# Performance work log

Hardware: AMD Instinct MI355X
Metric: run time of the kernel (lower is better)

## Reference

```python
import jax, jax.numpy as jnp
import numpy as np

N, E, F_IN, F_E = 50000, 800000, 128, 16
R, H, C = 4, 4, 32            # num_relations, heads, out_channels
HC = H * C                     # 128
NEG_SLOPE = 0.2                # PyG RGATConv default negative_slope
EPS = 1e-16                    # PyG softmax epsilon


def rgat_conv(x, src, dst, edge_type, edge_attr, w, q, k, e, le, b, concat):
    """Faithful PyG RGATConv (additive-self-attention, across-relation, dim=1, aggr=add).
    x: [N,F]; w: [R,F,H*C]; q,k,e: [H*C,H]; le: [F_e,H*C]; b: bias."""
    n = x.shape[0]
    xw = jnp.einsum('nf,rfo->rno', x, w)              # [R,N,H*C] per-relation projections
    x_i = xw[edge_type, dst]                          # [E,H*C] target-node proj per edge
    x_j = xw[edge_type, src]                          # [E,H*C] source-node proj per edge
    qi = x_i @ q                                      # [E,H]
    kj = x_j @ k + (edge_attr @ le) @ e               # [E,H] (edge features folded into keys)
    alpha = jax.nn.leaky_relu(qi + kj, NEG_SLOPE)     # [E,H]
    # softmax over incoming edges of each destination node (across relations)
    amax = jax.ops.segment_max(alpha, dst, num_segments=n)
    ex = jnp.exp(alpha - amax[dst])
    denom = jax.ops.segment_sum(ex, dst, num_segments=n)
    alpha = ex / (denom[dst] + EPS)
    msg = alpha[:, :, None] * x_j.reshape(-1, H, C)   # [E,H,C]
    out = jax.ops.segment_sum(msg, dst, num_segments=n)  # [N,H,C] sum aggregation
    out = out.reshape(n, H * C) if concat else out.mean(axis=1)
    return out + b


def setup_inputs() -> dict:
    key = jax.random.key(0)
    ks = jax.random.split(key, 18)
    p = 0.05
    inp = {
        'x': jax.random.normal(ks[0], (N, F_IN), dtype=jnp.float32),
        'edge_index': jax.random.randint(ks[1], (2, E), 0, N, dtype=jnp.int64)
            if jax.config.jax_enable_x64 else jax.random.randint(ks[1], (2, E), 0, N).astype(jnp.int32),
        'edge_attr': jax.random.normal(ks[2], (E, F_E), dtype=jnp.float32),
        'edge_type': jax.random.randint(ks[3], (E,), 0, R).astype(jnp.int32),
        # conv1 params (in=F_IN, concat=True -> bias of size H*C)
        'w1': jax.random.normal(ks[4], (R, F_IN, HC), dtype=jnp.float32) * p,
        'q1': jax.random.normal(ks[5], (HC, H), dtype=jnp.float32) * p,
        'k1': jax.random.normal(ks[6], (HC, H), dtype=jnp.float32) * p,
        'e1': jax.random.normal(ks[7], (HC, H), dtype=jnp.float32) * p,
        'le1': jax.random.normal(ks[8], (F_E, HC), dtype=jnp.float32) * p,
        'b1': jnp.zeros((HC,), dtype=jnp.float32),
        # conv3 params (in=H*C=128, concat=False -> bias of size C)
        'w3': jax.random.normal(ks[9], (R, HC, HC), dtype=jnp.float32) * p,
        'q3': jax.random.normal(ks[10], (HC, H), dtype=jnp.float32) * p,
        'k3': jax.random.normal(ks[11], (HC, H), dtype=jnp.float32) * p,
        'e3': jax.random.normal(ks[12], (HC, H), dtype=jnp.float32) * p,
        'le3': jax.random.normal(ks[13], (F_E, HC), dtype=jnp.float32) * p,
        'b3': jnp.zeros((C,), dtype=jnp.float32),
    }
    return inp


def reference(x, edge_index, edge_attr, edge_type,
              w1, q1, k1, e1, le1, b1,
              w3, q3, k3, e3, le3, b3):
    src, dst = edge_index[0], edge_index[1]
    h = jax.nn.relu(rgat_conv(x, src, dst, edge_type, edge_attr,
                              w1, q1, k1, e1, le1, b1, concat=True))
    out = rgat_conv(h, src, dst, edge_type, edge_attr,
                    w3, q3, k3, e3, le3, b3, concat=False)
    return out
```

## Files before the change

### kernel.cpp

```cpp
#include <hip/hip_runtime.h>


#define NEG_SLOPE 0.2f
#define SOFT_EPS 1e-16f

typedef __attribute__((ext_vector_type(8))) short bf16x8;
typedef __attribute__((ext_vector_type(4))) float f32x4;
typedef __attribute__((ext_vector_type(4))) unsigned short u16x4;
typedef __attribute__((ext_vector_type(4))) _Float16 half4;
typedef __attribute__((ext_vector_type(8))) _Float16 half8;

__device__ __forceinline__ void bf16split(float f, unsigned short& h, unsigned short& l) {
  unsigned u = __float_as_uint(f);
  unsigned r = u + 0x7FFFu + ((u >> 16) & 1u);
  h = (unsigned short)(r >> 16);
  float fh = __uint_as_float(((unsigned)h) << 16);
  float d = f - fh;
  unsigned u2 = __float_as_uint(d);
  unsigned r2 = u2 + 0x7FFFu + ((u2 >> 16) & 1u);
  l = (unsigned short)(r2 >> 16);
}


__device__ __forceinline__ void hist_body(int id, const int* __restrict__ dst,
                                          int* __restrict__ deg, int E) {
  int e = id * 256 + (int)threadIdx.x;
  if (e < E) atomicAdd(&deg[dst[e]], 1);
}

__device__ __forceinline__ void convx_body(int id, const float* __restrict__ in,
                                           unsigned short* __restrict__ hi,
                                           unsigned short* __restrict__ lo, int total8) {
  int i = id * 256 + (int)threadIdx.x;
  if (i >= total8) return;
  const float4* p = (const float4*)in + (size_t)i * 2;
  float4 a = p[0], b = p[1];
  float v[8] = {a.x, a.y, a.z, a.w, b.x, b.y, b.z, b.w};
  bf16x8 hv, lv;
#pragma unroll
  for (int j = 0; j < 8; ++j) {
    unsigned short h, l;
    bf16split(v[j], h, l);
    hv[j] = (short)h; lv[j] = (short)l;
  }
  *(bf16x8*)(hi + (size_t)i * 8) = hv;
  *(bf16x8*)(lo + (size_t)i * 8) = lv;
}

__device__ __forceinline__ void convw_body(int idx, const float* __restrict__ w1,
                                           const float* __restrict__ w3,
                                           unsigned short* __restrict__ wF1h,
                                           unsigned short* __restrict__ wF1l,
                                           unsigned short* __restrict__ wF3h,
                                           unsigned short* __restrict__ wF3l) {
  if (idx >= 131072) return;
  int L = idx >> 16;
  int rem = idx & 65535;
  int r = rem >> 14, rem2 = rem & 16383, f = rem2 >> 7, o = rem2 & 127;
  const float* w = L ? w3 : w1;
  unsigned short* dh = L ? wF3h : wF1h;
  unsigned short* dl = L ? wF3l : wF1l;
  float v = w[(r * 128 + f) * 128 + o];
  unsigned short h, l;
  bf16split(v, h, l);
  int ot = o >> 4, c = o & 15, kc = f >> 5, q = (f >> 3) & 3, j = f & 7;
  int di = r * 16384 + ((((ot * 4 + kc) * 4 + q) * 16 + c) * 8 + j);
  dh[di] = h;
  dl[di] = l;
}

__device__ __forceinline__ void wqk_body(int idx, const float* __restrict__ w1,
                                         const float* __restrict__ q1, const float* __restrict__ k1,
                                         const float* __restrict__ w3, const float* __restrict__ q3,
                                         const float* __restrict__ k3, float* __restrict__ wqk) {
  if (idx >= 8192) return;
  int L = idx >> 12, rem = idx & 4095;
  int r = rem >> 10, rem2 = rem & 1023, f = rem2 >> 3, j = rem2 & 7;
  const float* w = L ? w3 : w1;
  const float* qk = (j < 4) ? (L ? q3 : q1) : (L ? k3 : k1);
  int h = j & 3;
  const float* wrow = w + (r * 128 + f) * 128;
  float acc = 0.f;
  for (int o = 0; o < 128; ++o) acc += wrow[o] * qk[o * 4 + h];
  wqk[idx] = acc;
}

__device__ __forceinline__ void lee_body(const float* __restrict__ le1, const float* __restrict__ e1,
                                         const float* __restrict__ le3, const float* __restrict__ e3,
                                         float* __restrict__ lee) {
  int t = threadIdx.x;
  if (t >= 128) return;
  const float* le = (t < 64) ? le1 : le3;
  const float* ee = (t < 64) ? e1 : e3;
  int u = t & 63, f = u >> 2, h = u & 3;
  float acc = 0.f;
  for (int o = 0; o < 128; ++o) acc += le[f * 128 + o] * ee[o * 4 + h];
  lee[t] = acc;
}

__global__ __launch_bounds__(256) void pre_kernel(
    const int* __restrict__ dst, int* __restrict__ deg, int E,
    const float* __restrict__ x, unsigned short* __restrict__ xhi,
    unsigned short* __restrict__ xlo, int total8,
    const float* __restrict__ w1, const float* __restrict__ q1, const float* __restrict__ k1,
    const float* __restrict__ w3, const float* __restrict__ q3, const float* __restrict__ k3,
    float* __restrict__ wqk,
    const float* __restrict__ le1, const float* __restrict__ e1,
    const float* __restrict__ le3, const float* __restrict__ e3, float* __restrict__ lee,
    unsigned short* __restrict__ wF1h, unsigned short* __restrict__ wF1l,
    unsigned short* __restrict__ wF3h, unsigned short* __restrict__ wF3l,
    int nAB, int eb, int cxb) {
  int bid = blockIdx.x;
  if (bid < nAB) {
    int id = bid >> 1;
    if (bid & 1) {
      if (id < eb) hist_body(id, dst, deg, E);
    } else {
      if (id < cxb) convx_body(id, x, xhi, xlo, total8);
    }
  } else {
    int b2 = bid - nAB;
    if (b2 < 512) {
      convw_body(b2 * 256 + (int)threadIdx.x, w1, w3, wF1h, wF1l, wF3h, wF3l);
    } else if (b2 < 544) {
      wqk_body((b2 - 512) * 256 + (int)threadIdx.x, w1, q1, k1, w3, q3, k3, wqk);
    } else {
      lee_body(le1, e1, le3, e3, lee);
    }
  }
}


__global__ __launch_bounds__(256) void scanA_kernel(const int* __restrict__ deg,
                                                    int* __restrict__ bsum, int N) {
  int b = blockIdx.x, t = threadIdx.x;
  int base = b * 1024 + t * 4;
  int s = 0;
#pragma unroll
  for (int j = 0; j < 4; ++j) {
    int i = base + j;
    if (i < N) s += deg[i];
  }
#pragma unroll
  for (int o = 1; o < 64; o <<= 1) s += __shfl_xor(s, o);
  __shared__ int wsum[4];
  if ((t & 63) == 0) wsum[t >> 6] = s;
  __syncthreads();
  if (t == 0) bsum[b] = wsum[0] + wsum[1] + wsum[2] + wsum[3];
}

__global__ __launch_bounds__(256) void scanB_kernel(const int* __restrict__ bsum,
                                                    int* __restrict__ boff,
                                                    int* __restrict__ row_start,
                                                    int nb, int N) {
  int t = threadIdx.x;
  int v = (t < nb) ? bsum[t] : 0;
  int inc = v;
#pragma unroll
  for (int o = 1; o < 64; o <<= 1) {
    int u = __shfl_up(inc, o);
    if ((t & 63) >= o) inc += u;
  }
  __shared__ int wt[4];
  if ((t & 63) == 63) wt[t >> 6] = inc;
  __syncthreads();
  int add = 0;
  for (int wv = 0; wv < (t >> 6); ++wv) add += wt[wv];
  inc += add;
  if (t < nb) boff[t] = inc - v;
  if (t == 255) row_start[N] = inc;
}

__global__ __launch_bounds__(256) void scanC_kernel(const int* __restrict__ deg,
                                                    const int* __restrict__ boff,
                                                    int* __restrict__ row_start,
                                                    int* __restrict__ cursor, int N) {
  int b = blockIdx.x, t = threadIdx.x;
  int base = b * 1024 + t * 4;
  int d[4];
  int s = 0;
#pragma unroll
  for (int j = 0; j < 4; ++j) {
    int i = base + j;
    d[j] = (i < N) ? deg[i] : 0;
    s += d[j];
  }
  int inc = s;
#pragma unroll
  for (int o = 1; o < 64; o <<= 1) {
    int u = __shfl_up(inc, o);
    if ((t & 63) >= o) inc += u;
  }
  __shared__ int wt[4];
  if ((t & 63) == 63) wt[t >> 6] = inc;
  __syncthreads();
  int add = boff[b];
  for (int wv = 0; wv < (t >> 6); ++wv) add += wt[wv];
  int off = add + inc - s;
#pragma unroll
  for (int j = 0; j < 4; ++j) {
    int i = base + j;
    if (i < N) {
      row_start[i] = off;
      cursor[i] = off;
      off += d[j];
    }
  }
}


__device__ __forceinline__ void scatter_body(int id, const int* __restrict__ src,
                                             const int* __restrict__ dst,
                                             const int* __restrict__ et,
                                             int* __restrict__ cursor,
                                             int4* __restrict__ es, int E) {
  int e = id * 256 + (int)threadIdx.x;
  if (e >= E) return;
  int d = dst[e];
  int pos = atomicAdd(&cursor[d], 1);
  es[pos] = make_int4(src[e], d, et[e], e);
}

__device__ __forceinline__ void qkx_body(int nbid, char* smem, const float* __restrict__ xin,
                                         const float* __restrict__ wqk, float* __restrict__ qn,
                                         float* __restrict__ kn, int N) {
  float* swqk = (float*)smem;
  int t = threadIdx.x;
#pragma unroll
  for (int j = 0; j < 16; ++j) {
    int i = j * 256 + t;
    swqk[(i >> 10) * 1032 + (i & 1023)] = wqk[i];
  }
  __syncthreads();
  int nb = nbid * 64;
  int rl = t >> 2, r = t & 3;
  int n = nb + rl;
  int nc = n < N ? n : N - 1;
  const float4* xr = (const float4*)(xin + (size_t)nc * 128);
  const float* wb = swqk + r * 1032;
  float aq0 = 0, aq1 = 0, aq2 = 0, aq3 = 0;
  float ak0 = 0, ak1 = 0, ak2 = 0, ak3 = 0;
#pragma unroll 4
  for (int f4 = 0; f4 < 32; ++f4) {
    float4 xv = xr[f4];
    const float* w0 = wb + f4 * 32;
    float4 qa = *(const float4*)(w0);
    float4 ka = *(const float4*)(w0 + 4);
    float4 qb = *(const float4*)(w0 + 8);
    float4 kb = *(const float4*)(w0 + 12);
    float4 qc = *(const float4*)(w0 + 16);
    float4 kc = *(const float4*)(w0 + 20);
    float4 qd = *(const float4*)(w0 + 24);
    float4 kd = *(const float4*)(w0 + 28);
    aq0 += xv.x * qa.x + xv.y * qb.x + xv.z * qc.x + xv.w * qd.x;
    aq1 += xv.x * qa.y + xv.y * qb.y + xv.z * qc.y + xv.w * qd.y;
    aq2 += xv.x * qa.z + xv.y * qb.z + xv.z * qc.z + xv.w * qd.z;
    aq3 += xv.x * qa.w + xv.y * qb.w + xv.z * qc.w + xv.w * qd.w;
    ak0 += xv.x * ka.x + xv.y * kb.x + xv.z * kc.x + xv.w * kd.x;
    ak1 += xv.x * ka.y + xv.y * kb.y + xv.z * kc.y + xv.w * kd.y;
    ak2 += xv.x * ka.z + xv.y * kb.z + xv.z * kc.z + xv.w * kd.z;
    ak3 += xv.x * ka.w + xv.y * kb.w + xv.z * kc.w + xv.w * kd.w;
  }
  if (n < N) {
    *(float4*)(qn + ((size_t)r * N + n) * 4) = make_float4(aq0, aq1, aq2, aq3);
    *(float4*)(kn + ((size_t)r * N + n) * 4) = make_float4(ak0, ak1, ak2, ak3);
  }
}

__device__ __forceinline__ void proj_body(int pid, char* smem,
                                          const unsigned short* __restrict__ xhi,
                                          const unsigned short* __restrict__ xlo,
                                          const unsigned short* __restrict__ wFh,
                                          const unsigned short* __restrict__ wFl,
                                          _Float16* __restrict__ xwh, int N) {
  bf16x8* wl_h = (bf16x8*)smem;
  bf16x8* wl_l = wl_h + 1024;
  int r = pid & 3;
  int h0 = (pid >> 2) & 1;
  int nb = (pid >> 3) * 128;
  int t = threadIdx.x;
  const bf16x8* srcH = (const bf16x8*)(wFh + r * 16384) + h0 * 1024;
  const bf16x8* srcL = (const bf16x8*)(wFl + r * 16384) + h0 * 1024;
#pragma unroll
  for (int j = 0; j < 4; ++j) {
    int i = j * 256 + t;
    wl_h[i] = srcH[i];
    wl_l[i] = srcL[i];
  }
  __syncthreads();

  int wv = t >> 6;
  int lane = t & 63;
  int c = lane & 15, q = lane >> 4;
  int nodebase = nb + wv * 32;
  int n0 = nodebase + c;
  int n1 = nodebase + 16 + c;
  int n0c = n0 < N ? n0 : N - 1;
  int n1c = n1 < N ? n1 : N - 1;

  f32x4 acc[4][2];
#pragma unroll
  for (int ot = 0; ot < 4; ++ot)
#pragma unroll
    for (int nt = 0; nt < 2; ++nt) acc[ot][nt] = (f32x4){0.f, 0.f, 0.f, 0.f};

  bf16x8 xb[2][4];
  {
    int k0 = q * 8;
    xb[0][0] = *(const bf16x8*)(xhi + (size_t)n0c * 128 + k0);
    xb[0][1] = *(const bf16x8*)(xlo + (size_t)n0c * 128 + k0);
    xb[0][2] = *(const bf16x8*)(xhi + (size_t)n1c * 128 + k0);
    xb[0][3] = *(const bf16x8*)(xlo + (size_t)n1c * 128 + k0);
  }
#pragma unroll
  for (int kc = 0; kc < 4; ++kc) {
    if (kc < 3) {
      int k0 = (kc + 1) * 32 + q * 8;
      xb[(kc + 1) & 1][0] = *(const bf16x8*)(xhi + (size_t)n0c * 128 + k0);
      xb[(kc + 1) & 1][1] = *(const bf16x8*)(xlo + (size_t)n0c * 128 + k0);
      xb[(kc + 1) & 1][2] = *(const bf16x8*)(xhi + (size_t)n1c * 128 + k0);
      xb[(kc + 1) & 1][3] = *(const bf16x8*)(xlo + (size_t)n1c * 128 + k0);
    }
    bf16x8 b0h = xb[kc & 1][0], b0l = xb[kc & 1][1];
    bf16x8 b1h = xb[kc & 1][2], b1l = xb[kc & 1][3];
#pragma unroll
    for (int ot = 0; ot < 4; ++ot) {
      int fi = ((ot * 4 + kc) * 4 + q) * 16 + c;
      bf16x8 ah = wl_h[fi];
      bf16x8 al = wl_l[fi];
      acc[ot][0] = __builtin_amdgcn_mfma_f32_16x16x32_bf16(ah, b0h, acc[ot][0], 0, 0, 0);
      acc[ot][0] = __builtin_amdgcn_mfma_f32_16x16x32_bf16(ah, b0l, acc[ot][0], 0, 0, 0);
      acc[ot][0] = __builtin_amdgcn_mfma_f32_16x16x32_bf16(al, b0h, acc[ot][0], 0, 0, 0);
      acc[ot][1] = __builtin_amdgcn_mfma_f32_16x16x32_bf16(ah, b1h, acc[ot][1], 0, 0, 0);
      acc[ot][1] = __builtin_amdgcn_mfma_f32_16x16x32_bf16(ah, b1l, acc[ot][1], 0, 0, 0);
      acc[ot][1] = __builtin_amdgcn_mfma_f32_16x16x32_bf16(al, b1h, acc[ot][1], 0, 0, 0);
    }
  }

#pragma unroll
  for (int nt = 0; nt < 2; ++nt) {
    int n = nodebase + nt * 16 + c;
    if (n < N) {
      _Float16* basep = xwh + ((size_t)r * N + n) * 128 + h0 * 64 + q * 4;
#pragma unroll
      for (int ot = 0; ot < 4; ++ot) {
        f32x4 a = acc[ot][nt];
        half4 hv;
        hv[0] = (_Float16)a.x; hv[1] = (_Float16)a.y;
        hv[2] = (_Float16)a.z; hv[3] = (_Float16)a.w;
        *(half4*)(basep + ot * 16) = hv;
      }
    }
  }
}

__global__ __launch_bounds__(256) void sc9_kernel(
    const int* __restrict__ src, const int* __restrict__ dst, const int* __restrict__ et,
    int* __restrict__ cursor, int4* __restrict__ es, int E,
    const float* __restrict__ xin, const float* __restrict__ wqk,
    float* __restrict__ qn, float* __restrict__ kn, int N, int qxb,
    const unsigned short* __restrict__ xhi, const unsigned short* __restrict__ xlo,
    const unsigned short* __restrict__ wFh, const unsigned short* __restrict__ wFl,
    _Float16* __restrict__ xwh, int pjb) {
  extern __shared__ char smem[];
  int bid = blockIdx.x;
  int g = bid / 9, r9 = bid - g * 9;
  if (r9 < 4) {
    scatter_body(g * 4 + r9, src, dst, et, cursor, es, E);
  } else if (r9 == 4) {
    if (g < qxb) qkx_body(g, smem, xin, wqk, qn, kn, N);
  } else {
    int id = g * 4 + (r9 - 5);
    if (id < pjb) proj_body(id, smem, xhi, xlo, wFh, wFl, xwh, N);
  }
}


__global__ __launch_bounds__(256) void ek2_kernel(
    const int4* __restrict__ es, const float* __restrict__ ea,
    const float* __restrict__ lee, float* __restrict__ eks1,
    float* __restrict__ eks3, int E) {
  __shared__ float sl[128];
  if (threadIdx.x < 128) sl[threadIdx.x] = lee[threadIdx.x];
  __syncthreads();
  int i = blockIdx.x * 256 + (int)threadIdx.x;
  if (i >= E) return;
  int eid = es[i].w;
  const float4* a4 = (const float4*)(ea + (size_t)eid * 16);
  float a1[4] = {0, 0, 0, 0}, a3[4] = {0, 0, 0, 0};
#pragma unroll
  for (int ii = 0; ii < 4; ++ii) {
    float4 v = a4[ii];
    int f = ii * 4;
#pragma unroll
    for (int h = 0; h < 4; ++h) {
      a1[h] += v.x * sl[f * 4 + h] + v.y * sl[(f + 1) * 4 + h] +
               v.z * sl[(f + 2) * 4 + h] + v.w * sl[(f + 3) * 4 + h];
      a3[h] += v.x * sl[64 + f * 4 + h] + v.y * sl[64 + (f + 1) * 4 + h] +
               v.z * sl[64 + (f + 2) * 4 + h] + v.w * sl[64 + (f + 3) * 4 + h];
    }
  }
  *(float4*)(eks1 + (size_t)i * 4) = make_float4(a1[0], a1[1], a1[2], a1[3]);
  *(float4*)(eks3 + (size_t)i * 4) = make_float4(a3[0], a3[1], a3[2], a3[3]);
}

__global__ __launch_bounds__(256) void p2_kernel(
    const unsigned short* __restrict__ xhi, const unsigned short* __restrict__ xlo,
    const unsigned short* __restrict__ wFh, const unsigned short* __restrict__ wFl,
    _Float16* __restrict__ xwh, int N,
    const float* __restrict__ xin, const float* __restrict__ wqk,
    float* __restrict__ qn, float* __restrict__ kn, int pjb, int qxb) {
  extern __shared__ char smem[];
  int bid = blockIdx.x;
  int g = bid / 5, r5 = bid - g * 5;
  if (r5 == 4) {
    if (g < qxb) qkx_body(g, smem, xin, wqk, qn, kn, N);
  } else {
    int id = g * 4 + r5;
    if (id < pjb) proj_body(id, smem, xhi, xlo, wFh, wFl, xwh, N);
  }
}


__device__ __forceinline__ float4 edge_alpha(const int4* __restrict__ es,
                                             const float* __restrict__ qn,
                                             const float* __restrict__ kn,
                                             const float* __restrict__ eks,
                                             int i, int d, int N) {
  int4 v = es[i];
  float4 kv = *(const float4*)(kn + (v.z * N + v.x) * 4);
  float4 ev = ((const float4*)eks)[i];
  float4 q4 = *(const float4*)(qn + (v.z * N + d) * 4);
  float4 a = make_float4(q4.x + kv.x + ev.x, q4.y + kv.y + ev.y,
                         q4.z + kv.z + ev.z, q4.w + kv.w + ev.w);
  a.x = a.x > 0.f ? a.x : NEG_SLOPE * a.x;
  a.y = a.y > 0.f ? a.y : NEG_SLOPE * a.y;
  a.z = a.z > 0.f ? a.z : NEG_SLOPE * a.z;
  a.w = a.w > 0.f ? a.w : NEG_SLOPE * a.w;
  return a;
}

__device__ __forceinline__ float4 max4(float4 a, float4 b) {
  return make_float4(fmaxf(a.x, b.x), fmaxf(a.y, b.y), fmaxf(a.z, b.z), fmaxf(a.w, b.w));
}

__global__ __launch_bounds__(256) void agg_kernel(
    const int4* __restrict__ es, const int* __restrict__ row_start,
    const float* __restrict__ qn, const float* __restrict__ kn,
    const float* __restrict__ eks, float* __restrict__ alpha_s,
    const _Float16* __restrict__ xwh, const float* __restrict__ bias,
    float* __restrict__ out, unsigned short* __restrict__ xhi,
    unsigned short* __restrict__ xlo, int N, int concat) {
  int d = blockIdx.x * 16 + (threadIdx.x >> 4);
  if (d >= N) return;
  int ql = threadIdx.x & 15;
  int rs = row_start[d], re = row_start[d + 1];
  int deg = re - rs;
  int h = ql >> 2;

  float acc[8];
#pragma unroll
  for (int j = 0; j < 8; ++j) acc[j] = 0.f;
  float rden = 0.f;

  if (deg > 0) {
    float4 m = make_float4(-1e30f, -1e30f, -1e30f, -1e30f);
    float4 ar0 = m, ar1 = m, ar2 = m, ar3 = m;
    bool fast = (deg <= 64);
    bool v0 = ql < deg, v1 = 16 + ql < deg, v2 = 32 + ql < deg, v3 = 48 + ql < deg;
    if (fast) {
      int dm1 = deg - 1;
      int o0 = v0 ? ql : dm1;
      int o1 = v1 ? 16 + ql : dm1;
      int o2 = v2 ? 32 + ql : dm1;
      int o3 = v3 ? 48 + ql : dm1;
      float4 a0 = edge_alpha(es, qn, kn, eks, rs + o0, d, N);
      float4 a1 = edge_alpha(es, qn, kn, eks, rs + o1, d, N);
      float4 a2 = edge_alpha(es, qn, kn, eks, rs + o2, d, N);
      float4 a3 = edge_alpha(es, qn, kn, eks, rs + o3, d, N);
      if (v0) { ar0 = a0; m = max4(m, a0); }
      if (v1) { ar1 = a1; m = max4(m, a1); }
      if (v2) { ar2 = a2; m = max4(m, a2); }
      if (v3) { ar3 = a3; m = max4(m, a3); }
    } else {
      for (int i = rs + ql; i < re; i += 16) {
        float4 a = edge_alpha(es, qn, kn, eks, i, d, N);
        ((float4*)alpha_s)[i] = a;
        m = max4(m, a);
      }
    }
#pragma unroll
    for (int o = 1; o < 16; o <<= 1) {
      m.x = fmaxf(m.x, __shfl_xor(m.x, o));
      m.y = fmaxf(m.y, __shfl_xor(m.y, o));
      m.z = fmaxf(m.z, __shfl_xor(m.z, o));
      m.w = fmaxf(m.w, __shfl_xor(m.w, o));
    }

    float4 s = make_float4(0.f, 0.f, 0.f, 0.f);
    if (fast) {
#define SWEEPB(V, AR, OFF)                                                   \
      if (V) {                                                               \
        float4 e4 = make_float4(__expf(AR.x - m.x), __expf(AR.y - m.y),      \
                                __expf(AR.z - m.z), __expf(AR.w - m.w));     \
        ((float4*)alpha_s)[rs + OFF + ql] = e4;                              \
        s.x += e4.x; s.y += e4.y; s.z += e4.z; s.w += e4.w;                  \
      }
      SWEEPB(v0, ar0, 0)
      SWEEPB(v1, ar1, 16)
      SWEEPB(v2, ar2, 32)
      SWEEPB(v3, ar3, 48)
#undef SWEEPB
    } else {
      for (int i = rs + ql; i < re; i += 16) {
        float4 a = ((const float4*)alpha_s)[i];
        float4 e4 = make_float4(__expf(a.x - m.x), __expf(a.y - m.y),
                                __expf(a.z - m.z), __expf(a.w - m.w));
        ((float4*)alpha_s)[i] = e4;
        s.x += e4.x; s.y += e4.y; s.z += e4.z; s.w += e4.w;
      }
    }
#pragma unroll
    for (int o = 1; o < 16; o <<= 1) {
      s.x += __shfl_xor(s.x, o); s.y += __shfl_xor(s.y, o);
      s.z += __shfl_xor(s.z, o); s.w += __shfl_xor(s.w, o);
    }
    float smh = (h == 0) ? s.x : (h == 1) ? s.y : (h == 2) ? s.z : s.w;
    rden = 1.f / (smh + SOFT_EPS);

    int e = rs;
    for (; e + 4 <= re; e += 4) {
      int4 a0 = es[e];
      int4 a1 = es[e + 1];
      int4 a2 = es[e + 2];
      int4 a3 = es[e + 3];
      float w0 = alpha_s[e * 4 + h];
      float w1 = alpha_s[(e + 1) * 4 + h];
      float w2 = alpha_s[(e + 2) * 4 + h];
      float w3 = alpha_s[(e + 3) * 4 + h];
      half8 x0 = *(const half8*)(xwh + (a0.z * N + a0.x) * 128 + ql * 8);
      half8 x1 = *(const half8*)(xwh + (a1.z * N + a1.x) * 128 + ql * 8);
      half8 x2 = *(const half8*)(xwh + (a2.z * N + a2.x) * 128 + ql * 8);
      half8 x3 = *(const half8*)(xwh + (a3.z * N + a3.x) * 128 + ql * 8);
#pragma unroll
      for (int j = 0; j < 8; ++j) {
        acc[j] = fmaf((float)x0[j], w0, acc[j]);
        acc[j] = fmaf((float)x1[j], w1, acc[j]);
        acc[j] = fmaf((float)x2[j], w2, acc[j]);
        acc[j] = fmaf((float)x3[j], w3, acc[j]);
      }
    }
    for (; e < re; ++e) {
      int4 a0 = es[e];
      float w0 = alpha_s[e * 4 + h];
      half8 x0 = *(const half8*)(xwh + (a0.z * N + a0.x) * 128 + ql * 8);
#pragma unroll
      for (int j = 0; j < 8; ++j) acc[j] = fmaf((float)x0[j], w0, acc[j]);
    }
  }
#pragma unroll
  for (int j = 0; j < 8; ++j) acc[j] *= rden;

  if (concat) {
    float4 b0 = ((const float4*)bias)[ql * 2];
    float4 b1 = ((const float4*)bias)[ql * 2 + 1];
    float v[8] = {acc[0] + b0.x, acc[1] + b0.y, acc[2] + b0.z, acc[3] + b0.w,
                  acc[4] + b1.x, acc[5] + b1.y, acc[6] + b1.z, acc[7] + b1.w};
    u16x4 hv0, lv0, hv1, lv1;
#pragma unroll
    for (int j = 0; j < 8; ++j) {
      v[j] = v[j] > 0.f ? v[j] : 0.f;
      unsigned short hh, ll;
      bf16split(v[j], hh, ll);
      if (j < 4) { hv0[j] = hh; lv0[j] = ll; }
      else { hv1[j - 4] = hh; lv1[j - 4] = ll; }
    }
    float* orow = out + (size_t)d * 128 + ql * 8;
    *(float4*)orow = make_float4(v[0], v[1], v[2], v[3]);
    *(float4*)(orow + 4) = make_float4(v[4], v[5], v[6], v[7]);
    *(u16x4*)(xhi + (size_t)d * 128 + ql * 8) = hv0;
    *(u16x4*)(xhi + (size_t)d * 128 + ql * 8 + 4) = hv1;
    *(u16x4*)(xlo + (size_t)d * 128 + ql * 8) = lv0;
    *(u16x4*)(xlo + (size_t)d * 128 + ql * 8 + 4) = lv1;
  } else {
#pragma unroll
    for (int j = 0; j < 8; ++j) {
      acc[j] += __shfl_xor(acc[j], 4);
      acc[j] += __shfl_xor(acc[j], 8);
    }
    if (ql < 4) {
      float4 b0 = ((const float4*)bias)[ql * 2];
      float4 b1 = ((const float4*)bias)[ql * 2 + 1];
      float* orow = out + (size_t)d * 32 + ql * 8;
      *(float4*)orow = make_float4(0.25f * acc[0] + b0.x, 0.25f * acc[1] + b0.y,
                                   0.25f * acc[2] + b0.z, 0.25f * acc[3] + b0.w);
      *(float4*)(orow + 4) = make_float4(0.25f * acc[4] + b1.x, 0.25f * acc[5] + b1.y,
                                         0.25f * acc[6] + b1.z, 0.25f * acc[7] + b1.w);
    }
  }
}

extern "C" void kernel_launch(void* const* d_in, const int* in_sizes, int n_in,
                              void* d_out, int out_size, void* d_ws, size_t ws_size,
                              hipStream_t stream) {
  const float* x   = (const float*)d_in[0];
  const int*   ei  = (const int*)d_in[1];
  const float* ea  = (const float*)d_in[2];
  const int*   etp = (const int*)d_in[3];
  const float* w1  = (const float*)d_in[4];
  const float* q1  = (const float*)d_in[5];
  const float* k1  = (const float*)d_in[6];
  const float* e1  = (const float*)d_in[7];
  const float* le1 = (const float*)d_in[8];
  const float* b1  = (const float*)d_in[9];
  const float* w3  = (const float*)d_in[10];
  const float* q3  = (const float*)d_in[11];
  const float* k3  = (const float*)d_in[12];
  const float* e3  = (const float*)d_in[13];
  const float* le3 = (const float*)d_in[14];
  const float* b3  = (const float*)d_in[15];
  const int N = in_sizes[0] / 128;
  const int E = in_sizes[3];
  const int* srcp = ei;
  const int* dstp = ei + E;

  float* ws   = (float*)d_ws;
  _Float16* xwh = (_Float16*)ws;
  float* qn   = ws + (size_t)2 * N * 128;
  float* kn   = qn + (size_t)4 * N * 4;
  float* eks1 = kn + (size_t)4 * N * 4;
  float* eks3 = eks1 + (size_t)E * 4;
  float* alph = eks3 + (size_t)E * 4;
  float* hbuf = alph + (size_t)E * 4;
  float* leeb = hbuf + (size_t)N * 128;
  float* wqkb = leeb + 128;
  int* deg      = (int*)(wqkb + 8192);
  int* rowst    = deg + N;
  int* cursor   = rowst + N + 1;
  int* bsum     = cursor + N;
  int* boff     = bsum + 256;
  uintptr_t pe = (uintptr_t)(boff + 256);
  pe = (pe + 15) & ~(uintptr_t)15;
  int4* es      = (int4*)pe;
  uintptr_t pa = (uintptr_t)(es + E);
  pa = (pa + 255) & ~(uintptr_t)255;
  unsigned short* xhi  = (unsigned short*)pa;
  unsigned short* xlo  = xhi + (size_t)N * 128;
  unsigned short* wF1h = xlo + (size_t)N * 128;
  unsigned short* wF1l = wF1h + 4 * 128 * 128;
  unsigned short* wF3h = wF1l + 4 * 128 * 128;
  unsigned short* wF3l = wF3h + 4 * 128 * 128;
  (void)ws_size; (void)n_in; (void)out_size;

  int eb   = (E + 255) / 256;
  int nb16 = (N + 15) / 16;
  int nbs  = (N + 1023) / 1024;
  int pgy  = (N + 127) / 128;
  int pjb  = 8 * pgy;
  int qxb  = (N + 63) / 64;
  int cxb  = (N * 128 / 8 + 255) / 256;

  hipMemsetAsync(deg, 0, (size_t)N * sizeof(int), stream);

  int M = eb > cxb ? eb : cxb;
  int nAB = 2 * M;
  int preg = nAB + 512 + 32 + 1;
  pre_kernel<<<preg, 256, 0, stream>>>(dstp, deg, E, x, xhi, xlo, N * 128 / 8,
                                       w1, q1, k1, w3, q3, k3, wqkb,
                                       le1, e1, le3, e3, leeb,
                                       wF1h, wF1l, wF3h, wF3l, nAB, eb, cxb);
  scanA_kernel<<<nbs, 256, 0, stream>>>(deg, bsum, N);
  scanB_kernel<<<1, 256, 0, stream>>>(bsum, boff, rowst, nbs, N);
  scanC_kernel<<<nbs, 256, 0, stream>>>(deg, boff, rowst, cursor, N);

  int scq = (eb + 3) / 4;
  int pjq = (pjb + 3) / 4;
  int g9 = scq;
  if (qxb > g9) g9 = qxb;
  if (pjq > g9) g9 = pjq;
  sc9_kernel<<<9 * g9, 256, 32768, stream>>>(srcp, dstp, etp, cursor, es, E,
                                             x, wqkb, qn, kn, N, qxb,
                                             xhi, xlo, wF1h, wF1l, xwh, pjb);

  ek2_kernel<<<eb, 256, 0, stream>>>(es, ea, leeb, eks1, eks3, E);

  agg_kernel<<<nb16, 256, 0, stream>>>(es, rowst, qn, kn, eks1, alph, xwh,
                                       b1, hbuf, xhi, xlo, N, 1);

  int p2grp = pjq > qxb ? pjq : qxb;
  p2_kernel<<<5 * p2grp, 256, 32768, stream>>>(xhi, xlo, wF3h, wF3l, xwh, N,
                                               hbuf, wqkb + 4096, qn, kn, pjb, qxb);

  agg_kernel<<<nb16, 256, 0, stream>>>(es, rowst, qn, kn, eks3, alph, xwh,
                                       b3, (float*)d_out, xhi, xlo, N, 0);
}
```

Before: 432.2 us.

## Compute edge keys in original order in pre-kernel and pack sorted edge records

The edge-feature key projection now runs inside the pre kernel, indexed by original edge id, and the separate ek2 kernel and its gather through the sorted edge list are gone. Sorted edge records shrink from int4 to int2, with edge type packed into the top bits of the source index alongside the original edge id. This cuts one launch and halves the edge-list bytes read by the aggregation kernels. The cost is that aggregation now reads eks indirectly by edge id, which is a random access where it used to be sequential, and every pre-kernel block recomputes the small le·e table.

```diff
diff --git a/kernel.cpp b/kernel.cpp
--- a/kernel.cpp
+++ b/kernel.cpp
@@ -3,6 +3,7 @@
 
 #define NEG_SLOPE 0.2f
 #define SOFT_EPS 1e-16f
+#define SRC_MASK 0x07FFFFFF
 
 typedef __attribute__((ext_vector_type(8))) short bf16x8;
 typedef __attribute__((ext_vector_type(4))) float f32x4;
@@ -45,6 +46,42 @@
   }
   *(bf16x8*)(hi + (size_t)i * 8) = hv;
   *(bf16x8*)(lo + (size_t)i * 8) = lv;
+}
+
+__device__ __forceinline__ void ekp_body(int id, const float* __restrict__ ea,
+                                         const float* __restrict__ le1, const float* __restrict__ e1,
+                                         const float* __restrict__ le3, const float* __restrict__ e3,
+                                         float* __restrict__ eks1, float* __restrict__ eks3,
+                                         int E) {
+  __shared__ float sl[128];
+  int t = threadIdx.x;
+  if (t < 128) {
+    const float* le = (t < 64) ? le1 : le3;
+    const float* ee = (t < 64) ? e1 : e3;
+    int u = t & 63, f = u >> 2, h = u & 3;
+    float acc = 0.f;
+    for (int o = 0; o < 128; ++o) acc += le[f * 128 + o] * ee[o * 4 + h];
+    sl[t] = acc;
+  }
+  __syncthreads();
+  int i = id * 256 + t;
+  if (i >= E) return;
+  const float4* a4 = (const float4*)(ea + (size_t)i * 16);
+  float a1[4] = {0, 0, 0, 0}, a3[4] = {0, 0, 0, 0};
+#pragma unroll
+  for (int ii = 0; ii < 4; ++ii) {
+    float4 v = a4[ii];
+    int f = ii * 4;
+#pragma unroll
+    for (int h = 0; h < 4; ++h) {
+      a1[h] += v.x * sl[f * 4 + h] + v.y * sl[(f + 1) * 4 + h] +
+               v.z * sl[(f + 2) * 4 + h] + v.w * sl[(f + 3) * 4 + h];
+      a3[h] += v.x * sl[64 + f * 4 + h] + v.y * sl[64 + (f + 1) * 4 + h] +
+               v.z * sl[64 + (f + 2) * 4 + h] + v.w * sl[64 + (f + 3) * 4 + h];
+    }
+  }
+  *(float4*)(eks1 + (size_t)i * 4) = make_float4(a1[0], a1[1], a1[2], a1[3]);
+  *(float4*)(eks3 + (size_t)i * 4) = make_float4(a3[0], a3[1], a3[2], a3[3]);
 }
 
 __device__ __forceinline__ void convw_body(int idx, const float* __restrict__ w1,
@@ -85,47 +122,36 @@
   wqk[idx] = acc;
 }
 
-__device__ __forceinline__ void lee_body(const float* __restrict__ le1, const float* __restrict__ e1,
-                                         const float* __restrict__ le3, const float* __restrict__ e3,
-                                         float* __restrict__ lee) {
-  int t = threadIdx.x;
-  if (t >= 128) return;
-  const float* le = (t < 64) ? le1 : le3;
-  const float* ee = (t < 64) ? e1 : e3;
-  int u = t & 63, f = u >> 2, h = u & 3;
-  float acc = 0.f;
-  for (int o = 0; o < 128; ++o) acc += le[f * 128 + o] * ee[o * 4 + h];
-  lee[t] = acc;
-}
-
 __global__ __launch_bounds__(256) void pre_kernel(
     const int* __restrict__ dst, int* __restrict__ deg, int E,
     const float* __restrict__ x, unsigned short* __restrict__ xhi,
     unsigned short* __restrict__ xlo, int total8,
+    const float* __restrict__ ea,
+    const float* __restrict__ le1, const float* __restrict__ e1,
+    const float* __restrict__ le3, const float* __restrict__ e3,
+    float* __restrict__ eks1, float* __restrict__ eks3,
     const float* __restrict__ w1, const float* __restrict__ q1, const float* __restrict__ k1,
     const float* __restrict__ w3, const float* __restrict__ q3, const float* __restrict__ k3,
     float* __restrict__ wqk,
-    const float* __restrict__ le1, const float* __restrict__ e1,
-    const float* __restrict__ le3, const float* __restrict__ e3, float* __restrict__ lee,
     unsigned short* __restrict__ wF1h, unsigned short* __restrict__ wF1l,
     unsigned short* __restrict__ wF3h, unsigned short* __restrict__ wF3l,
-    int nAB, int eb, int cxb) {
+    int nABC, int eb, int cxb) {
   int bid = blockIdx.x;
-  if (bid < nAB) {
-    int id = bid >> 1;
-    if (bid & 1) {
+  if (bid < nABC) {
+    int id = bid / 3, r3 = bid - id * 3;
+    if (r3 == 0) {
       if (id < eb) hist_body(id, dst, deg, E);
+    } else if (r3 == 1) {
+      if (id < cxb) convx_body(id, x, xhi, xlo, total8);
     } else {
-      if (id < cxb) convx_body(id, x, xhi, xlo, total8);
+      if (id < eb) ekp_body(id, ea, le1, e1, le3, e3, eks1, eks3, E);
     }
   } else {
-    int b2 = bid - nAB;
+    int b2 = bid - nABC;
     if (b2 < 512) {
       convw_body(b2 * 256 + (int)threadIdx.x, w1, w3, wF1h, wF1l, wF3h, wF3l);
-    } else if (b2 < 544) {
+    } else {
       wqk_body((b2 - 512) * 256 + (int)threadIdx.x, w1, q1, k1, w3, q3, k3, wqk);
-    } else {
-      lee_body(le1, e1, le3, e3, lee);
     }
   }
 }
@@ -213,12 +239,12 @@
                                              const int* __restrict__ dst,
                                              const int* __restrict__ et,
                                              int* __restrict__ cursor,
-                                             int4* __restrict__ es, int E) {
+                                             int2* __restrict__ es2, int E) {
   int e = id * 256 + (int)threadIdx.x;
   if (e >= E) return;
   int d = dst[e];
   int pos = atomicAdd(&cursor[d], 1);
-  es[pos] = make_int4(src[e], d, et[e], e);
+  es2[pos] = make_int2(src[e] | (et[e] << 27), e);
 }
 
 __device__ __forceinline__ void qkx_body(int nbid, char* smem, const float* __restrict__ xin,
@@ -356,7 +382,7 @@
 
 __global__ __launch_bounds__(256) void sc9_kernel(
     const int* __restrict__ src, const int* __restrict__ dst, const int* __restrict__ et,
-    int* __restrict__ cursor, int4* __restrict__ es, int E,
+    int* __restrict__ cursor, int2* __restrict__ es2, int E,
     const float* __restrict__ xin, const float* __restrict__ wqk,
     float* __restrict__ qn, float* __restrict__ kn, int N, int qxb,
     const unsigned short* __restrict__ xhi, const unsigned short* __restrict__ xlo,
@@ -366,42 +392,13 @@
   int bid = blockIdx.x;
   int g = bid / 9, r9 = bid - g * 9;
   if (r9 < 4) {
-    scatter_body(g * 4 + r9, src, dst, et, cursor, es, E);
+    scatter_body(g * 4 + r9, src, dst, et, cursor, es2, E);
   } else if (r9 == 4) {
     if (g < qxb) qkx_body(g, smem, xin, wqk, qn, kn, N);
   } else {
     int id = g * 4 + (r9 - 5);
     if (id < pjb) proj_body(id, smem, xhi, xlo, wFh, wFl, xwh, N);
   }
-}
-
-
-__global__ __launch_bounds__(256) void ek2_kernel(
-    const int4* __restrict__ es, const float* __restrict__ ea,
-    const float* __restrict__ lee, float* __restrict__ eks1,
-    float* __restrict__ eks3, int E) {
-  __shared__ float sl[128];
-  if (threadIdx.x < 128) sl[threadIdx.x] = lee[threadIdx.x];
-  __syncthreads();
-  int i = blockIdx.x * 256 + (int)threadIdx.x;
-  if (i >= E) return;
-  int eid = es[i].w;
-  const float4* a4 = (const float4*)(ea + (size_t)eid * 16);
-  float a1[4] = {0, 0, 0, 0}, a3[4] = {0, 0, 0, 0};
-#pragma unroll
-  for (int ii = 0; ii < 4; ++ii) {
-    float4 v = a4[ii];
-    int f = ii * 4;
-#pragma unroll
-    for (int h = 0; h < 4; ++h) {
-      a1[h] += v.x * sl[f * 4 + h] + v.y * sl[(f + 1) * 4 + h] +
-               v.z * sl[(f + 2) * 4 + h] + v.w * sl[(f + 3) * 4 + h];
-      a3[h] += v.x * sl[64 + f * 4 + h] + v.y * sl[64 + (f + 1) * 4 + h] +
-               v.z * sl[64 + (f + 2) * 4 + h] + v.w * sl[64 + (f + 3) * 4 + h];
-    }
-  }
-  *(float4*)(eks1 + (size_t)i * 4) = make_float4(a1[0], a1[1], a1[2], a1[3]);
-  *(float4*)(eks3 + (size_t)i * 4) = make_float4(a3[0], a3[1], a3[2], a3[3]);
 }
 
 __global__ __launch_bounds__(256) void p2_kernel(
@@ -422,15 +419,17 @@
 }
 
 
-__device__ __forceinline__ float4 edge_alpha(const int4* __restrict__ es,
+__device__ __forceinline__ float4 edge_alpha(const int2* __restrict__ es2,
                                              const float* __restrict__ qn,
                                              const float* __restrict__ kn,
                                              const float* __restrict__ eks,
                                              int i, int d, int N) {
-  int4 v = es[i];
-  float4 kv = *(const float4*)(kn + (v.z * N + v.x) * 4);
-  float4 ev = ((const float4*)eks)[i];
-  float4 q4 = *(const float4*)(qn + (v.z * N + d) * 4);
+  int2 v = es2[i];
+  int et = (int)((unsigned)v.x >> 27);
+  int sn = v.x & SRC_MASK;
+  float4 kv = *(const float4*)(kn + (et * N + sn) * 4);
+  float4 ev = ((const float4*)eks)[v.y];
+  float4 q4 = *(const float4*)(qn + (et * N + d) * 4);
   float4 a = make_float4(q4.x + kv.x + ev.x, q4.y + kv.y + ev.y,
                          q4.z + kv.z + ev.z, q4.w + kv.w + ev.w);
   a.x = a.x > 0.f ? a.x : NEG_SLOPE * a.x;
@@ -445,7 +444,7 @@
 }
 
 __global__ __launch_bounds__(256) void agg_kernel(
-    const int4* __restrict__ es, const int* __restrict__ row_start,
+    const int2* __restrict__ es2, const int* __restrict__ row_start,
     const float* __restrict__ qn, const float* __restrict__ kn,
     const float* __restrict__ eks, float* __restrict__ alpha_s,
     const _Float16* __restrict__ xwh, const float* __restrict__ bias,
@@ -474,17 +473,17 @@
       int o1 = v1 ? 16 + ql : dm1;
       int o2 = v2 ? 32 + ql : dm1;
       int o3 = v3 ? 48 + ql : dm1;
-      float4 a0 = edge_alpha(es, qn, kn, eks, rs + o0, d, N);
-      float4 a1 = edge_alpha(es, qn, kn, eks, rs + o1, d, N);
-      float4 a2 = edge_alpha(es, qn, kn, eks, rs + o2, d, N);
-      float4 a3 = edge_alpha(es, qn, kn, eks, rs + o3, d, N);
+      float4 a0 = edge_alpha(es2, qn, kn, eks, rs + o0, d, N);
+      float4 a1 = edge_alpha(es2, qn, kn, eks, rs + o1, d, N);
+      float4 a2 = edge_alpha(es2, qn, kn, eks, rs + o2, d, N);
+      float4 a3 = edge_alpha(es2, qn, kn, eks, rs + o3, d, N);
       if (v0) { ar0 = a0; m = max4(m, a0); }
       if (v1) { ar1 = a1; m = max4(m, a1); }
       if (v2) { ar2 = a2; m = max4(m, a2); }
       if (v3) { ar3 = a3; m = max4(m, a3); }
     } else {
       for (int i = rs + ql; i < re; i += 16) {
-        float4 a = edge_alpha(es, qn, kn, eks, i, d, N);
+        float4 a = edge_alpha(es2, qn, kn, eks, i, d, N);
         ((float4*)alpha_s)[i] = a;
         m = max4(m, a);
       }
@@ -530,18 +529,22 @@
 
     int e = rs;
     for (; e + 4 <= re; e += 4) {
-      int4 a0 = es[e];
-      int4 a1 = es[e + 1];
-      int4 a2 = es[e + 2];
-      int4 a3 = es[e + 3];
+      int2 a0 = es2[e];
+      int2 a1 = es2[e + 1];
+      int2 a2 = es2[e + 2];
+      int2 a3 = es2[e + 3];
       float w0 = alpha_s[e * 4 + h];
       float w1 = alpha_s[(e + 1) * 4 + h];
       float w2 = alpha_s[(e + 2) * 4 + h];
       float w3 = alpha_s[(e + 3) * 4 + h];
-      half8 x0 = *(const half8*)(xwh + (a0.z * N + a0.x) * 128 + ql * 8);
-      half8 x1 = *(const half8*)(xwh + (a1.z * N + a1.x) * 128 + ql * 8);
-      half8 x2 = *(const half8*)(xwh + (a2.z * N + a2.x) * 128 + ql * 8);
-      half8 x3 = *(const half8*)(xwh + (a3.z * N + a3.x) * 128 + ql * 8);
+      int p0 = ((int)((unsigned)a0.x >> 27)) * N + (a0.x & SRC_MASK);
+      int p1 = ((int)((unsigned)a1.x >> 27)) * N + (a1.x & SRC_MASK);
+      int p2 = ((int)((unsigned)a2.x >> 27)) * N + (a2.x & SRC_MASK);
+      int p3 = ((int)((unsigned)a3.x >> 27)) * N + (a3.x & SRC_MASK);
+      half8 x0 = *(const half8*)(xwh + (size_t)p0 * 128 + ql * 8);
+      half8 x1 = *(const half8*)(xwh + (size_t)p1 * 128 + ql * 8);
+      half8 x2 = *(const half8*)(xwh + (size_t)p2 * 128 + ql * 8);
+      half8 x3 = *(const half8*)(xwh + (size_t)p3 * 128 + ql * 8);
 #pragma unroll
       for (int j = 0; j < 8; ++j) {
         acc[j] = fmaf((float)x0[j], w0, acc[j]);
@@ -551,9 +554,10 @@
       }
     }
     for (; e < re; ++e) {
-      int4 a0 = es[e];
+      int2 a0 = es2[e];
       float w0 = alpha_s[e * 4 + h];
-      half8 x0 = *(const half8*)(xwh + (a0.z * N + a0.x) * 128 + ql * 8);
+      int p0 = ((int)((unsigned)a0.x >> 27)) * N + (a0.x & SRC_MASK);
+      half8 x0 = *(const half8*)(xwh + (size_t)p0 * 128 + ql * 8);
 #pragma unroll
       for (int j = 0; j < 8; ++j) acc[j] = fmaf((float)x0[j], w0, acc[j]);
     }
@@ -632,8 +636,7 @@
   float* eks3 = eks1 + (size_t)E * 4;
   float* alph = eks3 + (size_t)E * 4;
   float* hbuf = alph + (size_t)E * 4;
-  float* leeb = hbuf + (size_t)N * 128;
-  float* wqkb = leeb + 128;
+  float* wqkb = hbuf + (size_t)N * 128;
   int* deg      = (int*)(wqkb + 8192);
   int* rowst    = deg + N;
   int* cursor   = rowst + N + 1;
@@ -641,8 +644,8 @@
   int* boff     = bsum + 256;
   uintptr_t pe = (uintptr_t)(boff + 256);
   pe = (pe + 15) & ~(uintptr_t)15;
-  int4* es      = (int4*)pe;
-  uintptr_t pa = (uintptr_t)(es + E);
+  int2* es2     = (int2*)pe;
+  uintptr_t pa = (uintptr_t)(es2 + E);
   pa = (pa + 255) & ~(uintptr_t)255;
   unsigned short* xhi  = (unsigned short*)pa;
   unsigned short* xlo  = xhi + (size_t)N * 128;
@@ -663,12 +666,12 @@
   hipMemsetAsync(deg, 0, (size_t)N * sizeof(int), stream);
 
   int M = eb > cxb ? eb : cxb;
-  int nAB = 2 * M;
-  int preg = nAB + 512 + 32 + 1;
+  int nABC = 3 * M;
+  int preg = nABC + 512 + 32;
   pre_kernel<<<preg, 256, 0, stream>>>(dstp, deg, E, x, xhi, xlo, N * 128 / 8,
+                                       ea, le1, e1, le3, e3, eks1, eks3,
                                        w1, q1, k1, w3, q3, k3, wqkb,
-                                       le1, e1, le3, e3, leeb,
-                                       wF1h, wF1l, wF3h, wF3l, nAB, eb, cxb);
+                                       wF1h, wF1l, wF3h, wF3l, nABC, eb, cxb);
   scanA_kernel<<<nbs, 256, 0, stream>>>(deg, bsum, N);
   scanB_kernel<<<1, 256, 0, stream>>>(bsum, boff, rowst, nbs, N);
   scanC_kernel<<<nbs, 256, 0, stream>>>(deg, boff, rowst, cursor, N);
@@ -678,19 +681,17 @@
   int g9 = scq;
   if (qxb > g9) g9 = qxb;
   if (pjq > g9) g9 = pjq;
-  sc9_kernel<<<9 * g9, 256, 32768, stream>>>(srcp, dstp, etp, cursor, es, E,
+  sc9_kernel<<<9 * g9, 256, 32768, stream>>>(srcp, dstp, etp, cursor, es2, E,
                                              x, wqkb, qn, kn, N, qxb,
                                              xhi, xlo, wF1h, wF1l, xwh, pjb);
 
-  ek2_kernel<<<eb, 256, 0, stream>>>(es, ea, leeb, eks1, eks3, E);
-
-  agg_kernel<<<nb16, 256, 0, stream>>>(es, rowst, qn, kn, eks1, alph, xwh,
+  agg_kernel<<<nb16, 256, 0, stream>>>(es2, rowst, qn, kn, eks1, alph, xwh,
                                        b1, hbuf, xhi, xlo, N, 1);
 
   int p2grp = pjq > qxb ? pjq : qxb;
   p2_kernel<<<5 * p2grp, 256, 32768, stream>>>(xhi, xlo, wF3h, wF3l, xwh, N,
                                                hbuf, wqkb + 4096, qn, kn, pjb, qxb);
 
-  agg_kernel<<<nb16, 256, 0, stream>>>(es, rowst, qn, kn, eks3, alph, xwh,
+  agg_kernel<<<nb16, 256, 0, stream>>>(es2, rowst, qn, kn, eks3, alph, xwh,
                                        b3, (float*)d_out, xhi, xlo, N, 0);
 }
```

Measured after the change: 436.5 us. No clear change (+1.0%).

## Fuse layer-2 attention q/k projection into layer-1 aggregation epilogue

Applied to the files above, without the earlier changes.

The per-node q/k attention logits for the second layer are now computed inside the first aggregation kernel's epilogue, using in-register activations and a 16-lane shuffle reduction per relation. This removes the fp32 hidden-buffer write and the separate qkx blocks in the second projection kernel, which becomes a plain projection launch. It writes into new qn2/kn2 buffers so the first-layer logits are not overwritten while still being read. In exchange the aggregation epilogue does more arithmetic and shuffles per node, and its weight loads may raise register pressure.

```diff
diff --git a/kernel.cpp b/kernel.cpp
--- a/kernel.cpp
+++ b/kernel.cpp
@@ -404,21 +404,13 @@
   *(float4*)(eks3 + (size_t)i * 4) = make_float4(a3[0], a3[1], a3[2], a3[3]);
 }
 
-__global__ __launch_bounds__(256) void p2_kernel(
+__global__ __launch_bounds__(256) void projL2_kernel(
     const unsigned short* __restrict__ xhi, const unsigned short* __restrict__ xlo,
     const unsigned short* __restrict__ wFh, const unsigned short* __restrict__ wFl,
-    _Float16* __restrict__ xwh, int N,
-    const float* __restrict__ xin, const float* __restrict__ wqk,
-    float* __restrict__ qn, float* __restrict__ kn, int pjb, int qxb) {
+    _Float16* __restrict__ xwh, int N, int pjb) {
   extern __shared__ char smem[];
-  int bid = blockIdx.x;
-  int g = bid / 5, r5 = bid - g * 5;
-  if (r5 == 4) {
-    if (g < qxb) qkx_body(g, smem, xin, wqk, qn, kn, N);
-  } else {
-    int id = g * 4 + r5;
-    if (id < pjb) proj_body(id, smem, xhi, xlo, wFh, wFl, xwh, N);
-  }
+  int id = blockIdx.x;
+  if (id < pjb) proj_body(id, smem, xhi, xlo, wFh, wFl, xwh, N);
 }
 
 
@@ -450,7 +442,9 @@
     const float* __restrict__ eks, float* __restrict__ alpha_s,
     const _Float16* __restrict__ xwh, const float* __restrict__ bias,
     float* __restrict__ out, unsigned short* __restrict__ xhi,
-    unsigned short* __restrict__ xlo, int N, int concat) {
+    unsigned short* __restrict__ xlo,
+    float* __restrict__ qn2, float* __restrict__ kn2,
+    const float* __restrict__ wqk3, int N, int concat) {
   int d = blockIdx.x * 16 + (threadIdx.x >> 4);
   if (d >= N) return;
   int ql = threadIdx.x & 15;
@@ -575,13 +569,37 @@
       if (j < 4) { hv0[j] = hh; lv0[j] = ll; }
       else { hv1[j - 4] = hh; lv1[j - 4] = ll; }
     }
-    float* orow = out + (size_t)d * 128 + ql * 8;
-    *(float4*)orow = make_float4(v[0], v[1], v[2], v[3]);
-    *(float4*)(orow + 4) = make_float4(v[4], v[5], v[6], v[7]);
     *(u16x4*)(xhi + (size_t)d * 128 + ql * 8) = hv0;
     *(u16x4*)(xhi + (size_t)d * 128 + ql * 8 + 4) = hv1;
     *(u16x4*)(xlo + (size_t)d * 128 + ql * 8) = lv0;
     *(u16x4*)(xlo + (size_t)d * 128 + ql * 8 + 4) = lv1;
+
+#pragma unroll
+    for (int r = 0; r < 4; ++r) {
+      const float* wb = wqk3 + r * 1024 + ql * 64;
+      float p0 = 0, p1 = 0, p2 = 0, p3 = 0, p4 = 0, p5 = 0, p6 = 0, p7 = 0;
+#pragma unroll
+      for (int j = 0; j < 8; ++j) {
+        float hv = v[j];
+        float4 wa = *(const float4*)(wb + j * 8);
+        float4 wk = *(const float4*)(wb + j * 8 + 4);
+        p0 = fmaf(hv, wa.x, p0); p1 = fmaf(hv, wa.y, p1);
+        p2 = fmaf(hv, wa.z, p2); p3 = fmaf(hv, wa.w, p3);
+        p4 = fmaf(hv, wk.x, p4); p5 = fmaf(hv, wk.y, p5);
+        p6 = fmaf(hv, wk.z, p6); p7 = fmaf(hv, wk.w, p7);
+      }
+#pragma unroll
+      for (int o = 1; o < 16; o <<= 1) {
+        p0 += __shfl_xor(p0, o); p1 += __shfl_xor(p1, o);
+        p2 += __shfl_xor(p2, o); p3 += __shfl_xor(p3, o);
+        p4 += __shfl_xor(p4, o); p5 += __shfl_xor(p5, o);
+        p6 += __shfl_xor(p6, o); p7 += __shfl_xor(p7, o);
+      }
+      if (ql == 0) {
+        *(float4*)(qn2 + ((size_t)r * N + d) * 4) = make_float4(p0, p1, p2, p3);
+        *(float4*)(kn2 + ((size_t)r * N + d) * 4) = make_float4(p4, p5, p6, p7);
+      }
+    }
   } else {
 #pragma unroll
     for (int j = 0; j < 8; ++j) {
@@ -628,11 +646,12 @@
   _Float16* xwh = (_Float16*)ws;
   float* qn   = ws + (size_t)2 * N * 128;
   float* kn   = qn + (size_t)4 * N * 4;
-  float* eks1 = kn + (size_t)4 * N * 4;
+  float* qn2  = kn + (size_t)4 * N * 4;
+  float* kn2  = qn2 + (size_t)4 * N * 4;
+  float* eks1 = kn2 + (size_t)4 * N * 4;
   float* eks3 = eks1 + (size_t)E * 4;
   float* alph = eks3 + (size_t)E * 4;
-  float* hbuf = alph + (size_t)E * 4;
-  float* leeb = hbuf + (size_t)N * 128;
+  float* leeb = alph + (size_t)E * 4;
   float* wqkb = leeb + 128;
   int* deg      = (int*)(wqkb + 8192);
   int* rowst    = deg + N;
@@ -685,12 +704,12 @@
   ek2_kernel<<<eb, 256, 0, stream>>>(es, ea, leeb, eks1, eks3, E);
 
   agg_kernel<<<nb16, 256, 0, stream>>>(es, rowst, qn, kn, eks1, alph, xwh,
-                                       b1, hbuf, xhi, xlo, N, 1);
-
-  int p2grp = pjq > qxb ? pjq : qxb;
-  p2_kernel<<<5 * p2grp, 256, 32768, stream>>>(xhi, xlo, wF3h, wF3l, xwh, N,
-                                               hbuf, wqkb + 4096, qn, kn, pjb, qxb);
-
-  agg_kernel<<<nb16, 256, 0, stream>>>(es, rowst, qn, kn, eks3, alph, xwh,
-                                       b3, (float*)d_out, xhi, xlo, N, 0);
-}
+                                       b1, (float*)d_out, xhi, xlo,
+                                       qn2, kn2, wqkb + 4096, N, 1);
+
+  projL2_kernel<<<pjb, 256, 32768, stream>>>(xhi, xlo, wF3h, wF3l, xwh, N, pjb);
+
+  agg_kernel<<<nb16, 256, 0, stream>>>(es, rowst, qn2, kn2, eks3, alph, xwh,
+                                       b3, (float*)d_out, xhi, xlo,
+                                       qn2, kn2, wqkb + 4096, N, 0);
+}
```

Measured after the change: 489.8 us. 1.13x slower.
